# Performance work log

Measured on AMD Instinct MI355X. Metric: run time of the kernel, lower is better.

The kernel has to match this reference:

```python
import jax, jax.numpy as jnp
import numpy as np

N_NODES = 50000
N_EDGES = 800000
N_GRAPHS = 64
NEG_SLOPE = 0.2  # PyG GATConv default negative_slope


def gat_conv(x, src, dst, W, att_src, att_dst, bias, heads, out_ch, concat):
    """PyG-style GATConv (eval mode, self-loops already in src/dst)."""
    N = x.shape[0]
    h = (x @ W).reshape(N, heads, out_ch)            # [N,H,C]
    a_s = jnp.sum(h * att_src, axis=-1)              # [N,H]
    a_d = jnp.sum(h * att_dst, axis=-1)              # [N,H]
    e = jax.nn.leaky_relu(a_s[src] + a_d[dst], NEG_SLOPE)  # [E,H]
    # segment softmax over incoming edges of each dst node
    m = jax.ops.segment_max(e, dst, num_segments=N)
    m = jnp.where(jnp.isfinite(m), m, 0.0)
    ex = jnp.exp(e - m[dst])
    denom = jax.ops.segment_sum(ex, dst, num_segments=N)
    alpha = ex / (denom[dst] + 1e-16)                # [E,H]
    out = jax.ops.segment_sum(alpha[:, :, None] * h[src], dst, num_segments=N)  # [N,H,C]
    out = out.reshape(N, heads * out_ch) if concat else out.mean(axis=1)
    return out + bias


def setup_inputs() -> dict:
    key = jax.random.key(0)
    ks = jax.random.split(key, 12)
    x = jax.random.normal(ks[0], (N_NODES, 5), dtype=jnp.float32)
    edge_index = jax.random.randint(ks[1], (2, N_EDGES), 0, N_NODES, dtype=jnp.int64)
    batch = jnp.sort(jax.random.randint(ks[2], (N_NODES,), 0, N_GRAPHS, dtype=jnp.int64))
    def glorot(k, shape):
        fan_in, fan_out = shape[0], shape[-1]
        s = jnp.sqrt(6.0 / (fan_in + fan_out))
        return jax.random.uniform(k, shape, jnp.float32, -s, s)
    return {
        "x": x,
        "edge_index": edge_index,
        "batch": batch,
        "W1": glorot(ks[3], (5, 256)),
        "att_src1": glorot(ks[4], (4, 64)),
        "att_dst1": glorot(ks[5], (4, 64)),
        "b1": jnp.zeros((256,), jnp.float32),
        "W2": glorot(ks[6], (256, 64)),
        "att_src2": glorot(ks[7], (1, 64)),
        "att_dst2": glorot(ks[8], (1, 64)),
        "b2": jnp.zeros((64,), jnp.float32),
        "lin_W": glorot(ks[9], (64, 2)),
        "lin_b": jnp.zeros((2,), jnp.float32),
    }


def reference(x, edge_index, batch, W1, att_src1, att_dst1, b1,
              W2, att_src2, att_dst2, b2, lin_W, lin_b):
    N = x.shape[0]
    loops = jnp.arange(N, dtype=edge_index.dtype)
    src = jnp.concatenate([edge_index[0], loops])
    dst = jnp.concatenate([edge_index[1], loops])
    h = jax.nn.relu(gat_conv(x, src, dst, W1, att_src1, att_dst1, b1, 4, 64, True))
    h = jax.nn.relu(gat_conv(h, src, dst, W2, att_src2, att_dst2, b2, 1, 64, False))
    # global mean pool over graphs
    sums = jax.ops.segment_sum(h, batch, num_segments=N_GRAPHS)          # [G,64]
    cnts = jax.ops.segment_sum(jnp.ones((N,), h.dtype), batch, num_segments=N_GRAPHS)
    pooled = sums / jnp.maximum(cnts, 1.0)[:, None]
    return pooled @ lin_W + lin_b
```

## Files before the change

kernel.cpp:

```cpp
#include <hip/hip_runtime.h>
#include <math.h>

#define N_NODES 50000
#define N_EDGES 800000
#define N_GRAPHS 64
#define NEG_SLOPE 0.2f
#define SCAN_BS 512
#define SCAN_NB ((N_NODES + SCAN_BS - 1) / SCAN_BS)
#define N_REP 64
#define ZERO_INT4 ((N_NODES * 4 + N_REP * N_GRAPHS * 64 * 4) / 16)

typedef __attribute__((ext_vector_type(8))) short short8;
typedef __attribute__((ext_vector_type(4))) float f32x4;

__device__ __forceinline__ float lrelu(float x) { return x > 0.f ? x : NEG_SLOPE * x; }

__device__ __forceinline__ unsigned short f2bf(float f) {
    union { float f; unsigned int u; } v; v.f = f;
    unsigned int r = (v.u + 0x7fffu + ((v.u >> 16) & 1u)) >> 16;
    return (unsigned short)r;
}
__device__ __forceinline__ float bf2f(unsigned short b) {
    union { unsigned int u; float f; } v; v.u = ((unsigned int)b) << 16;
    return v.f;
}
__device__ __forceinline__ float bfLO(unsigned int u) {
    union { unsigned int u; float f; } v; v.u = u << 16;
    return v.f;
}
__device__ __forceinline__ float bfHI(unsigned int u) {
    union { unsigned int u; float f; } v; v.u = u & 0xffff0000u;
    return v.f;
}

__device__ __forceinline__ int lower_bound_i(const int* __restrict__ a, int n, int v) {
    int lo = 0, hi = n;
    while (lo < hi) { int m = (lo + hi) >> 1; if (a[m] < v) lo = m + 1; else hi = m; }
    return lo;
}

__global__ void k_zero(int4* __restrict__ p) {
    int i = blockIdx.x * blockDim.x + threadIdx.x;
    if (i < ZERO_INT4) p[i] = make_int4(0, 0, 0, 0);
}

__global__ void k_countrank(const int* __restrict__ dst, int* __restrict__ cnt,
                            int* __restrict__ rank) {
    const int base = (blockIdx.x * blockDim.x + threadIdx.x) * 4;
    if (base + 4 <= N_EDGES) {
        int4 d4 = *(const int4*)(dst + base);
        int4 r;
        r.x = atomicAdd(&cnt[d4.x], 1);
        r.y = atomicAdd(&cnt[d4.y], 1);
        r.z = atomicAdd(&cnt[d4.z], 1);
        r.w = atomicAdd(&cnt[d4.w], 1);
        *(int4*)(rank + base) = r;
    } else {
        for (int e = base; e < N_EDGES; ++e) rank[e] = atomicAdd(&cnt[dst[e]], 1);
    }
}

__global__ void k_scatter(const int* __restrict__ src, const int* __restrict__ dst,
                          const int* __restrict__ rank, const int* __restrict__ row_start,
                          int* __restrict__ csr_src) {
    const int base = (blockIdx.x * blockDim.x + threadIdx.x) * 4;
    if (base + 4 <= N_EDGES) {
        int4 d4 = *(const int4*)(dst + base);
        int4 s4 = *(const int4*)(src + base);
        int4 r4 = *(const int4*)(rank + base);
        csr_src[row_start[d4.x] + r4.x] = s4.x;
        csr_src[row_start[d4.y] + r4.y] = s4.y;
        csr_src[row_start[d4.z] + r4.z] = s4.z;
        csr_src[row_start[d4.w] + r4.w] = s4.w;
    } else {
        for (int e = base; e < N_EDGES; ++e)
            csr_src[row_start[dst[e]] + rank[e]] = src[e];
    }
}

__global__ __launch_bounds__(SCAN_BS) void k_scan1(const int* __restrict__ cnt,
                                                   int* __restrict__ local_pref,
                                                   int* __restrict__ blk_sum) {
    const int t = threadIdx.x;
    const int gid = blockIdx.x * SCAN_BS + t;
    const int lane = t & 63, w = t >> 6;
    int v = (gid < N_NODES) ? cnt[gid] : 0;
    int x = v;
#pragma unroll
    for (int off = 1; off < 64; off <<= 1) {
        int y = __shfl_up(x, off, 64);
        if (lane >= off) x += y;
    }
    __shared__ int wsum[SCAN_BS / 64];
    __shared__ int wpre[SCAN_BS / 64];
    if (lane == 63) wsum[w] = x;
    __syncthreads();
    if (t == 0) {
        int run = 0;
#pragma unroll
        for (int i = 0; i < SCAN_BS / 64; ++i) { wpre[i] = run; run += wsum[i]; }
    }
    __syncthreads();
    int excl = x - v + wpre[w];
    if (gid < N_NODES) local_pref[gid] = excl;
    if (t == SCAN_BS - 1) blk_sum[blockIdx.x] = excl + v;
}

__global__ __launch_bounds__(128) void k_scan2(const int* __restrict__ blk_sum,
                                               int* __restrict__ blk_base,
                                               int* __restrict__ row_start) {
    const int t = threadIdx.x;
    const int lane = t & 63;
    int v = (t < SCAN_NB) ? blk_sum[t] : 0;
    int x = v;
#pragma unroll
    for (int off = 1; off < 64; off <<= 1) {
        int y = __shfl_up(x, off, 64);
        if (lane >= off) x += y;
    }
    __shared__ int wsum0;
    if (t == 63) wsum0 = x;
    __syncthreads();
    int excl = x - v + ((t >= 64) ? wsum0 : 0);
    if (t < SCAN_NB) blk_base[t] = excl;
    if (t == 127) row_start[N_NODES] = excl + v;
}

__global__ __launch_bounds__(SCAN_BS) void k_scan3(const int* __restrict__ local_pref,
                                                   const int* __restrict__ blk_base,
                                                   int* __restrict__ row_start) {
    const int gid = blockIdx.x * SCAN_BS + threadIdx.x;
    if (gid < N_NODES) row_start[gid] = local_pref[gid] + blk_base[blockIdx.x];
}

__global__ __launch_bounds__(256) void k_gemm1(const float* __restrict__ x,
                                               const float* __restrict__ W1,
                                               const float* __restrict__ att_s,
                                               const float* __restrict__ att_d,
                                               float4* __restrict__ a_s,
                                               float4* __restrict__ a_d) {
    __shared__ float Ws[5 * 256];
    const int t = threadIdx.x;
    for (int i = t; i < 5 * 256; i += 256) Ws[i] = W1[i];
    __syncthreads();
    const int wave = t >> 6, lane = t & 63;
    const int n = blockIdx.x * 4 + wave;
    if (n >= N_NODES) return;
    float x0 = x[n * 5 + 0], x1 = x[n * 5 + 1], x2 = x[n * 5 + 2],
          x3 = x[n * 5 + 3], x4 = x[n * 5 + 4];
    float vs[4], vd[4];
#pragma unroll
    for (int hd = 0; hd < 4; ++hd) {
        const int c = hd * 64 + lane;
        float h = x0 * Ws[c] + x1 * Ws[256 + c] + x2 * Ws[512 + c] +
                  x3 * Ws[768 + c] + x4 * Ws[1024 + c];
        vs[hd] = h * att_s[c];
        vd[hd] = h * att_d[c];
    }
#pragma unroll
    for (int off = 32; off; off >>= 1) {
#pragma unroll
        for (int hd = 0; hd < 4; ++hd) {
            vs[hd] += __shfl_xor(vs[hd], off, 64);
            vd[hd] += __shfl_xor(vd[hd], off, 64);
        }
    }
    if (lane == 0) {
        a_s[n] = make_float4(vs[0], vs[1], vs[2], vs[3]);
        a_d[n] = make_float4(vd[0], vd[1], vd[2], vd[3]);
    }
}

__global__ __launch_bounds__(256) void k_agg1(const float* __restrict__ x,
                                              const float* __restrict__ W1,
                                              const float4* __restrict__ asv,
                                              const float4* __restrict__ adv,
                                              const int* __restrict__ row_start,
                                              const int* __restrict__ csr_src,
                                              const float* __restrict__ b1,
                                              unsigned short* __restrict__ out1rm) {
    __shared__ float hand[4][4][24];
    const int t = threadIdx.x;
    const int wave = t >> 6, lane = t & 63;
    const int grp = lane >> 4, l16 = lane & 15;
    const int d = blockIdx.x * 16 + wave * 4 + grp;

    float w1r[4][5], bias[4];
#pragma unroll
    for (int h = 0; h < 4; ++h) {
#pragma unroll
        for (int i = 0; i < 5; ++i) w1r[h][i] = W1[i * 256 + h * 64 + lane];
        bias[h] = b1[h * 64 + lane];
    }

    const int beg = row_start[d], end = row_start[d + 1];
    const float4 ad = adv[d];

    float den[4] = {0.f, 0.f, 0.f, 0.f};
    float xw[4][5];
#pragma unroll
    for (int h = 0; h < 4; ++h)
#pragma unroll
        for (int i = 0; i < 5; ++i) xw[h][i] = 0.f;

    for (int cb = beg; cb < end; cb += 16) {
        const int j = cb + l16;
        if (j < end) {
            const int s = csr_src[j];
            const float4 a = asv[s];
            float w[4];
            w[0] = __expf(lrelu(a.x + ad.x));
            w[1] = __expf(lrelu(a.y + ad.y));
            w[2] = __expf(lrelu(a.z + ad.z));
            w[3] = __expf(lrelu(a.w + ad.w));
            const float* xp = x + (size_t)s * 5;
            float xv[5];
#pragma unroll
            for (int i = 0; i < 5; ++i) xv[i] = xp[i];
#pragma unroll
            for (int h = 0; h < 4; ++h) {
                den[h] += w[h];
#pragma unroll
                for (int i = 0; i < 5; ++i) xw[h][i] += w[h] * xv[i];
            }
        }
    }

#pragma unroll
    for (int off = 1; off < 16; off <<= 1) {
#pragma unroll
        for (int h = 0; h < 4; ++h) {
            den[h] += __shfl_xor(den[h], off, 64);
#pragma unroll
            for (int i = 0; i < 5; ++i) xw[h][i] += __shfl_xor(xw[h][i], off, 64);
        }
    }

    {
        const float4 as = asv[d];
        float w[4];
        w[0] = __expf(lrelu(as.x + ad.x));
        w[1] = __expf(lrelu(as.y + ad.y));
        w[2] = __expf(lrelu(as.z + ad.z));
        w[3] = __expf(lrelu(as.w + ad.w));
        const float* xp = x + (size_t)d * 5;
        float xv[5];
#pragma unroll
        for (int i = 0; i < 5; ++i) xv[i] = xp[i];
#pragma unroll
        for (int h = 0; h < 4; ++h) {
            den[h] += w[h];
#pragma unroll
            for (int i = 0; i < 5; ++i) xw[h][i] += w[h] * xv[i];
        }
    }

    if (l16 == 0) {
#pragma unroll
        for (int h = 0; h < 4; ++h) hand[wave][grp][h] = den[h];
#pragma unroll
        for (int h = 0; h < 4; ++h)
#pragma unroll
            for (int i = 0; i < 5; ++i) hand[wave][grp][4 + h * 5 + i] = xw[h][i];
    }
    __syncthreads();

#pragma unroll
    for (int n = 0; n < 4; ++n) {
        const int dn = blockIdx.x * 16 + wave * 4 + n;
        unsigned short* op = out1rm + (size_t)dn * 256;
#pragma unroll
        for (int h = 0; h < 4; ++h) {
            const float dh = hand[wave][n][h] + 1e-16f;
            float hh = hand[wave][n][4 + h * 5 + 0] * w1r[h][0]
                     + hand[wave][n][4 + h * 5 + 1] * w1r[h][1]
                     + hand[wave][n][4 + h * 5 + 2] * w1r[h][2]
                     + hand[wave][n][4 + h * 5 + 3] * w1r[h][3]
                     + hand[wave][n][4 + h * 5 + 4] * w1r[h][4];
            op[h * 64 + lane] = f2bf(fmaxf(hh / dh + bias[h], 0.f));
        }
    }
}

__global__ __launch_bounds__(256) void k_gemm2(const unsigned short* __restrict__ in,
                                               const float* __restrict__ W2,
                                               const float* __restrict__ att_s2,
                                               const float* __restrict__ att_d2,
                                               unsigned short* __restrict__ h2b,
                                               float* __restrict__ a_s2,
                                               float* __restrict__ a_d2) {
    __shared__ unsigned short lW[16384];
    const int t = threadIdx.x;
    for (int idx = t; idx < 16384; idx += 256) {
        int j = idx & 7, c16 = (idx >> 3) & 15, tt = (idx >> 7) & 3,
            g = (idx >> 9) & 3, s = idx >> 11;
        int k = 32 * s + 8 * g + j, c = 16 * tt + c16;
        lW[idx] = f2bf(W2[k * 64 + c]);
    }
    __syncthreads();
    const int wave = t >> 6, lane = t & 63;
    const int g = lane >> 4, c16 = lane & 15;
    const int nb = blockIdx.x * 64 + wave * 16;
    if (nb >= N_NODES) return;

    f32x4 acc[4];
#pragma unroll
    for (int i = 0; i < 4; ++i) acc[i] = (f32x4){0.f, 0.f, 0.f, 0.f};

    const unsigned short* arow = in + (size_t)(nb + c16) * 256;
#pragma unroll
    for (int s = 0; s < 8; ++s) {
        short8 a = *reinterpret_cast<const short8*>(arow + 32 * s + 8 * g);
#pragma unroll
        for (int tt = 0; tt < 4; ++tt) {
            short8 b = *reinterpret_cast<const short8*>(
                lW + ((((s * 4 + g) * 4 + tt) * 16 + c16) << 3));
            acc[tt] = __builtin_amdgcn_mfma_f32_16x16x32_bf16(a, b, acc[tt], 0, 0, 0);
        }
    }

    float attS[4], attD[4];
#pragma unroll
    for (int tt = 0; tt < 4; ++tt) {
        attS[tt] = att_s2[16 * tt + c16];
        attD[tt] = att_d2[16 * tt + c16];
    }
#pragma unroll
    for (int r = 0; r < 4; ++r) {
        const int node = nb + g * 4 + r;
        const bool ok = node < N_NODES;
        float vs = 0.f, vd = 0.f;
#pragma unroll
        for (int tt = 0; tt < 4; ++tt) {
            float v = acc[tt][r];
            if (ok) h2b[(size_t)node * 64 + 16 * tt + c16] = f2bf(v);
            vs += v * attS[tt];
            vd += v * attD[tt];
        }
#pragma unroll
        for (int off = 1; off < 16; off <<= 1) {
            vs += __shfl_xor(vs, off, 64);
            vd += __shfl_xor(vd, off, 64);
        }
        if (ok && c16 == 0) { a_s2[node] = vs; a_d2[node] = vd; }
    }
}

__global__ __launch_bounds__(256) void k_agg2(const unsigned short* __restrict__ h2b,
                                              const float* __restrict__ as_,
                                              const float* __restrict__ ad_,
                                              const int* __restrict__ row_start,
                                              const int* __restrict__ csr_src,
                                              const float* __restrict__ b2,
                                              const int* __restrict__ batch,
                                              float* __restrict__ sums) {
    const unsigned int* h2u = (const unsigned int*)h2b;
    const int wave = threadIdx.x >> 6, lane = threadIdx.x & 63;
    const int m = lane & 31, half = lane >> 5;
    const int d = blockIdx.x * 4 + wave;
    if (d >= N_NODES) return;
    const int beg = row_start[d], end = row_start[d + 1];
    const float adl = ad_[d];

    float den;
    float accx = 0.f, accy = 0.f;
    {
        float w = __expf(lrelu(as_[d] + adl));
        den = (lane == 0) ? w : 0.f;
        if (half == 0) {
            unsigned int v = h2u[(size_t)d * 32 + m];
            accx = w * bfLO(v); accy = w * bfHI(v);
        }
    }
    for (int c = beg; c < end; c += 64) {
        int rem = end - c; if (rem > 64) rem = 64;
        int sreg = 0;
        float wr = 0.f;
        if (lane < rem) {
            sreg = csr_src[c + lane];
            wr = __expf(lrelu(as_[sreg] + adl));
            den += wr;
        }
        int e = 0;
        for (; e + 8 <= rem; e += 8) {
            int e0 = e + half, e1 = e + 2 + half, e2 = e + 4 + half, e3 = e + 6 + half;
            int s0 = __shfl(sreg, e0, 64), s1 = __shfl(sreg, e1, 64);
            int s2 = __shfl(sreg, e2, 64), s3 = __shfl(sreg, e3, 64);
            unsigned int v0 = h2u[(size_t)s0 * 32 + m];
            unsigned int v1 = h2u[(size_t)s1 * 32 + m];
            unsigned int v2 = h2u[(size_t)s2 * 32 + m];
            unsigned int v3 = h2u[(size_t)s3 * 32 + m];
            float w0 = __shfl(wr, e0, 64), w1 = __shfl(wr, e1, 64);
            float w2 = __shfl(wr, e2, 64), w3 = __shfl(wr, e3, 64);
            accx += w0 * bfLO(v0); accy += w0 * bfHI(v0);
            accx += w1 * bfLO(v1); accy += w1 * bfHI(v1);
            accx += w2 * bfLO(v2); accy += w2 * bfHI(v2);
            accx += w3 * bfLO(v3); accy += w3 * bfHI(v3);
        }
        for (; e + 2 <= rem; e += 2) {
            int eh = e + half;
            int s = __shfl(sreg, eh, 64);
            float w = __shfl(wr, eh, 64);
            unsigned int v = h2u[(size_t)s * 32 + m];
            accx += w * bfLO(v); accy += w * bfHI(v);
        }
        if (e < rem) {
            int s = __shfl(sreg, e, 64);
            float w = __shfl(wr, e, 64);
            if (half == 0) {
                unsigned int v = h2u[(size_t)s * 32 + m];
                accx += w * bfLO(v); accy += w * bfHI(v);
            }
        }
    }
    accx += __shfl_xor(accx, 32, 64);
    accy += __shfl_xor(accy, 32, 64);
#pragma unroll
    for (int off = 32; off; off >>= 1) den += __shfl_xor(den, off, 64);
    if (half == 0) {
        float inv = 1.0f / (den + 1e-16f);
        float v0 = fmaxf(accx * inv + b2[2 * m], 0.f);
        float v1 = fmaxf(accy * inv + b2[2 * m + 1], 0.f);
        const int rep = blockIdx.x & (N_REP - 1);
        float* sb = sums + (size_t)rep * (N_GRAPHS * 64) + batch[d] * 64;
        atomicAdd(&sb[2 * m], v0);
        atomicAdd(&sb[2 * m + 1], v1);
    }
}

__global__ __launch_bounds__(64) void k_final(const float* __restrict__ sums,
                                              const int* __restrict__ batch,
                                              const float* __restrict__ linW,
                                              const float* __restrict__ linb,
                                              float* __restrict__ out) {
    const int g = blockIdx.x;
    const int lane = threadIdx.x;
    float s = 0.f;
#pragma unroll 8
    for (int r = 0; r < N_REP; ++r)
        s += sums[(size_t)r * (N_GRAPHS * 64) + g * 64 + lane];
    int beg = lower_bound_i(batch, N_NODES, g);
    int end = lower_bound_i(batch, N_NODES, g + 1);
    float val = s / fmaxf((float)(end - beg), 1.0f);
    float v0 = val * linW[lane * 2 + 0];
    float v1 = val * linW[lane * 2 + 1];
#pragma unroll
    for (int off = 32; off; off >>= 1) {
        v0 += __shfl_xor(v0, off, 64);
        v1 += __shfl_xor(v1, off, 64);
    }
    if (lane == 0) {
        out[g * 2 + 0] = v0 + linb[0];
        out[g * 2 + 1] = v1 + linb[1];
    }
}

extern "C" void kernel_launch(void* const* d_in, const int* in_sizes, int n_in,
                              void* d_out, int out_size, void* d_ws, size_t ws_size,
                              hipStream_t stream) {
    const float* x    = (const float*)d_in[0];
    const int*   ei   = (const int*)d_in[1];
    const int*   bat  = (const int*)d_in[2];
    const float* W1   = (const float*)d_in[3];
    const float* as1  = (const float*)d_in[4];
    const float* ad1  = (const float*)d_in[5];
    const float* b1   = (const float*)d_in[6];
    const float* W2   = (const float*)d_in[7];
    const float* as2  = (const float*)d_in[8];
    const float* ad2  = (const float*)d_in[9];
    const float* b2   = (const float*)d_in[10];
    const float* linW = (const float*)d_in[11];
    const float* linb = (const float*)d_in[12];
    float* out = (float*)d_out;

    const int* src = ei;
    const int* dst = ei + N_EDGES;

    char* w = (char*)d_ws;
    unsigned short* out1rm = (unsigned short*)w; w += (size_t)N_NODES * 256 * 2;
    float4* a_s1 = (float4*)w; w += (size_t)N_NODES * 16;
    float4* a_d1 = (float4*)w; w += (size_t)N_NODES * 16;
    unsigned short* h2b = (unsigned short*)w; w += (size_t)N_NODES * 64 * 2;
    float* a_s2  = (float*)w; w += (size_t)N_NODES * 4;
    float* a_d2  = (float*)w; w += (size_t)N_NODES * 4;
    int* counts  = (int*)w;   w += (size_t)N_NODES * 4;
    float* sums  = (float*)w; w += (size_t)N_REP * N_GRAPHS * 64 * 4;
    int* row_start = (int*)w; w += (size_t)(N_NODES + 64) * 4;
    int* lpref     = (int*)w; w += (size_t)N_NODES * 4;
    int* rank      = (int*)w; w += (size_t)N_EDGES * 4;
    int* csr_src   = (int*)w; w += (size_t)N_EDGES * 4;
    int* blk_sum   = (int*)w; w += 128 * 4;
    int* blk_base  = (int*)w; w += 128 * 4;

    k_zero<<<(ZERO_INT4 + 255) / 256, 256, 0, stream>>>((int4*)counts);
    k_countrank<<<(N_EDGES / 4 + 255) / 256, 256, 0, stream>>>(dst, counts, rank);
    k_scan1<<<SCAN_NB, SCAN_BS, 0, stream>>>(counts, lpref, blk_sum);
    k_scan2<<<1, 128, 0, stream>>>(blk_sum, blk_base, row_start);
    k_scan3<<<SCAN_NB, SCAN_BS, 0, stream>>>(lpref, blk_base, row_start);
    k_scatter<<<(N_EDGES / 4 + 255) / 256, 256, 0, stream>>>(src, dst, rank, row_start, csr_src);

    k_gemm1<<<(N_NODES + 3) / 4, 256, 0, stream>>>(x, W1, as1, ad1, a_s1, a_d1);
    k_agg1<<<N_NODES / 16, 256, 0, stream>>>(x, W1, a_s1, a_d1, row_start, csr_src, b1, out1rm);
    k_gemm2<<<(N_NODES + 63) / 64, 256, 0, stream>>>(out1rm, W2, as2, ad2, h2b, a_s2, a_d2);
    k_agg2<<<(N_NODES + 3) / 4, 256, 0, stream>>>(h2b, a_s2, a_d2, row_start, csr_src, b2,
                                                  bat, sums);
    k_final<<<N_GRAPHS, 64, 0, stream>>>(sums, bat, linW, linb, out);
}
```

Before: 208.1 us.

## Partition CSR scatter by dst range and use half-wave per node in agg2

The scatter kernel now splits edges into slices and assigns each block one of 8 destination-node ranges. Every block rescans its slice but writes only edges whose dst falls in its range, which keeps its writes in a narrower region of csr_src for better locality. The cost is reading each edge slice eight times. The second-layer aggregation now handles two nodes per wave, one per half-wave, and stages edge source/weight pairs in shared memory instead of using shuffles, to reduce idle lanes on low-degree nodes.

```diff
diff --git a/kernel.cpp b/kernel.cpp
--- a/kernel.cpp
+++ b/kernel.cpp
@@ -9,6 +9,8 @@
 #define SCAN_NB ((N_NODES + SCAN_BS - 1) / SCAN_BS)
 #define N_REP 64
 #define ZERO_INT4 ((N_NODES * 4 + N_REP * N_GRAPHS * 64 * 4) / 16)
+#define SCAT_GRID 2048
+#define NPX (N_NODES / 8)
 
 typedef __attribute__((ext_vector_type(8))) short short8;
 typedef __attribute__((ext_vector_type(4))) float f32x4;
@@ -60,21 +62,22 @@
     }
 }
 
-__global__ void k_scatter(const int* __restrict__ src, const int* __restrict__ dst,
-                          const int* __restrict__ rank, const int* __restrict__ row_start,
-                          int* __restrict__ csr_src) {
-    const int base = (blockIdx.x * blockDim.x + threadIdx.x) * 4;
-    if (base + 4 <= N_EDGES) {
-        int4 d4 = *(const int4*)(dst + base);
-        int4 s4 = *(const int4*)(src + base);
-        int4 r4 = *(const int4*)(rank + base);
-        csr_src[row_start[d4.x] + r4.x] = s4.x;
-        csr_src[row_start[d4.y] + r4.y] = s4.y;
-        csr_src[row_start[d4.z] + r4.z] = s4.z;
-        csr_src[row_start[d4.w] + r4.w] = s4.w;
-    } else {
-        for (int e = base; e < N_EDGES; ++e)
-            csr_src[row_start[dst[e]] + rank[e]] = src[e];
+__global__ __launch_bounds__(256) void k_scatter(const int* __restrict__ src,
+                                                 const int* __restrict__ dst,
+                                                 const int* __restrict__ rank,
+                                                 const int* __restrict__ row_start,
+                                                 int* __restrict__ csr_src) {
+    const int r = blockIdx.x & 7;
+    const int slice = blockIdx.x >> 3;
+    const int lo = r * NPX;
+    const int per = (N_EDGES + (SCAT_GRID / 8) - 1) / (SCAT_GRID / 8);
+    const int e0 = slice * per;
+    const int e1 = min(e0 + per, N_EDGES);
+    for (int e = e0 + threadIdx.x; e < e1; e += 256) {
+        int d = dst[e];
+        if ((unsigned)(d - lo) < (unsigned)NPX) {
+            csr_src[row_start[d] + rank[e]] = src[e];
+        }
     }
 }
 
@@ -346,7 +349,7 @@
     }
 }
 
-__global__ __launch_bounds__(256) void k_agg2(const unsigned short* __restrict__ h2b,
+__global__ __launch_bounds__(256) void k_agg2(const unsigned int* __restrict__ h2u,
                                               const float* __restrict__ as_,
                                               const float* __restrict__ ad_,
                                               const int* __restrict__ row_start,
@@ -354,78 +357,60 @@
                                               const float* __restrict__ b2,
                                               const int* __restrict__ batch,
                                               float* __restrict__ sums) {
-    const unsigned int* h2u = (const unsigned int*)h2b;
-    const int wave = threadIdx.x >> 6, lane = threadIdx.x & 63;
-    const int m = lane & 31, half = lane >> 5;
-    const int d = blockIdx.x * 4 + wave;
-    if (d >= N_NODES) return;
+    __shared__ int2 ew[4][2][32];
+    const int t = threadIdx.x;
+    const int wid = t >> 6, lane = t & 63;
+    const int g = lane >> 5, m = lane & 31;
+    const int d = blockIdx.x * 8 + wid * 2 + g;
     const int beg = row_start[d], end = row_start[d + 1];
     const float adl = ad_[d];
 
-    float den;
-    float accx = 0.f, accy = 0.f;
-    {
-        float w = __expf(lrelu(as_[d] + adl));
-        den = (lane == 0) ? w : 0.f;
-        if (half == 0) {
-            unsigned int v = h2u[(size_t)d * 32 + m];
-            accx = w * bfLO(v); accy = w * bfHI(v);
-        }
-    }
-    for (int c = beg; c < end; c += 64) {
-        int rem = end - c; if (rem > 64) rem = 64;
-        int sreg = 0;
-        float wr = 0.f;
-        if (lane < rem) {
-            sreg = csr_src[c + lane];
-            wr = __expf(lrelu(as_[sreg] + adl));
-            den += wr;
+    float den = 0.f, accx = 0.f, accy = 0.f;
+    for (int c = beg; c < end; c += 32) {
+        int rem = end - c; if (rem > 32) rem = 32;
+        if (m < rem) {
+            int s = csr_src[c + m];
+            float w = __expf(lrelu(as_[s] + adl));
+            den += w;
+            ew[wid][g][m] = make_int2(s, __float_as_int(w));
         }
         int e = 0;
-        for (; e + 8 <= rem; e += 8) {
-            int e0 = e + half, e1 = e + 2 + half, e2 = e + 4 + half, e3 = e + 6 + half;
-            int s0 = __shfl(sreg, e0, 64), s1 = __shfl(sreg, e1, 64);
-            int s2 = __shfl(sreg, e2, 64), s3 = __shfl(sreg, e3, 64);
-            unsigned int v0 = h2u[(size_t)s0 * 32 + m];
-            unsigned int v1 = h2u[(size_t)s1 * 32 + m];
-            unsigned int v2 = h2u[(size_t)s2 * 32 + m];
-            unsigned int v3 = h2u[(size_t)s3 * 32 + m];
-            float w0 = __shfl(wr, e0, 64), w1 = __shfl(wr, e1, 64);
-            float w2 = __shfl(wr, e2, 64), w3 = __shfl(wr, e3, 64);
+        for (; e + 4 <= rem; e += 4) {
+            int2 p0 = ew[wid][g][e],     p1 = ew[wid][g][e + 1];
+            int2 p2 = ew[wid][g][e + 2], p3 = ew[wid][g][e + 3];
+            unsigned int v0 = h2u[(size_t)p0.x * 32 + m];
+            unsigned int v1 = h2u[(size_t)p1.x * 32 + m];
+            unsigned int v2 = h2u[(size_t)p2.x * 32 + m];
+            unsigned int v3 = h2u[(size_t)p3.x * 32 + m];
+            float w0 = __int_as_float(p0.y), w1 = __int_as_float(p1.y);
+            float w2 = __int_as_float(p2.y), w3 = __int_as_float(p3.y);
             accx += w0 * bfLO(v0); accy += w0 * bfHI(v0);
             accx += w1 * bfLO(v1); accy += w1 * bfHI(v1);
             accx += w2 * bfLO(v2); accy += w2 * bfHI(v2);
             accx += w3 * bfLO(v3); accy += w3 * bfHI(v3);
         }
-        for (; e + 2 <= rem; e += 2) {
-            int eh = e + half;
-            int s = __shfl(sreg, eh, 64);
-            float w = __shfl(wr, eh, 64);
-            unsigned int v = h2u[(size_t)s * 32 + m];
+        for (; e < rem; ++e) {
+            int2 p = ew[wid][g][e];
+            unsigned int v = h2u[(size_t)p.x * 32 + m];
+            float w = __int_as_float(p.y);
             accx += w * bfLO(v); accy += w * bfHI(v);
         }
-        if (e < rem) {
-            int s = __shfl(sreg, e, 64);
-            float w = __shfl(wr, e, 64);
-            if (half == 0) {
-                unsigned int v = h2u[(size_t)s * 32 + m];
-                accx += w * bfLO(v); accy += w * bfHI(v);
-            }
-        }
-    }
-    accx += __shfl_xor(accx, 32, 64);
-    accy += __shfl_xor(accy, 32, 64);
-#pragma unroll
-    for (int off = 32; off; off >>= 1) den += __shfl_xor(den, off, 64);
-    if (half == 0) {
-        float inv = 1.0f / (den + 1e-16f);
-        float v0 = fmaxf(accx * inv + b2[2 * m], 0.f);
-        float v1 = fmaxf(accy * inv + b2[2 * m + 1], 0.f);
-        const int rep = blockIdx.x & (N_REP - 1);
-        float* sb = sums + (size_t)rep * (N_GRAPHS * 64) + batch[d] * 64;
-        atomicAdd(&sb[2 * m], v0);
-        atomicAdd(&sb[2 * m + 1], v1);
-    }
+    }
+#pragma unroll
+    for (int off = 16; off; off >>= 1) den += __shfl_xor(den, off, 64);
+    {
+        float w = __expf(lrelu(as_[d] + adl));
+        den += w;
+        unsigned int v = h2u[(size_t)d * 32 + m];
+        accx += w * bfLO(v); accy += w * bfHI(v);
+    }
+    float inv = 1.0f / (den + 1e-16f);
+    float v0 = fmaxf(accx * inv + b2[2 * m], 0.f);
+    float v1 = fmaxf(accy * inv + b2[2 * m + 1], 0.f);
+    const int rep = ((blockIdx.x << 3) + (wid << 1) + g) & (N_REP - 1);
+    float* sb = sums + (size_t)rep * (N_GRAPHS * 64) + batch[d] * 64;
+    atomicAdd(&sb[2 * m], v0);
+    atomicAdd(&sb[2 * m + 1], v1);
 }
 
 __global__ __launch_bounds__(64) void k_final(const float* __restrict__ sums,
@@ -497,12 +482,12 @@
     k_scan1<<<SCAN_NB, SCAN_BS, 0, stream>>>(counts, lpref, blk_sum);
     k_scan2<<<1, 128, 0, stream>>>(blk_sum, blk_base, row_start);
     k_scan3<<<SCAN_NB, SCAN_BS, 0, stream>>>(lpref, blk_base, row_start);
-    k_scatter<<<(N_EDGES / 4 + 255) / 256, 256, 0, stream>>>(src, dst, rank, row_start, csr_src);
+    k_scatter<<<SCAT_GRID, 256, 0, stream>>>(src, dst, rank, row_start, csr_src);
 
     k_gemm1<<<(N_NODES + 3) / 4, 256, 0, stream>>>(x, W1, as1, ad1, a_s1, a_d1);
     k_agg1<<<N_NODES / 16, 256, 0, stream>>>(x, W1, a_s1, a_d1, row_start, csr_src, b1, out1rm);
     k_gemm2<<<(N_NODES + 63) / 64, 256, 0, stream>>>(out1rm, W2, as2, ad2, h2b, a_s2, a_d2);
-    k_agg2<<<(N_NODES + 3) / 4, 256, 0, stream>>>(h2b, a_s2, a_d2, row_start, csr_src, b2,
-                                                  bat, sums);
+    k_agg2<<<N_NODES / 8, 256, 0, stream>>>((const unsigned int*)h2b, a_s2, a_d2,
+                                            row_start, csr_src, b2, bat, sums);
     k_final<<<N_GRAPHS, 64, 0, stream>>>(sums, bat, linW, linb, out);
 }
```

New measurement: 205.8 us. About the same (-1.1%).
